# Optimization experiments

Measured on AMD Instinct MI355X. Metric: run time of the kernel, lower is better.

The kernel has to match this reference:

```python
import jax, jax.numpy as jnp
import numpy as np

B, L, D, H, NL, F = 64, 197, 768, 12, 12, 3072
HD = D // H
EPS = 1e-6


def setup_inputs() -> dict:
    key = jax.random.key(0)
    ks = jax.random.split(key, 8)
    s = 0.02  # init std, matches nn.Parameter normal_(std=0.02) / xavier-ish scale
    def n(k, shape, scale=s):
        return jax.random.normal(k, shape, jnp.float32) * scale
    return {
        "x": jax.random.normal(ks[0], (B, L, D), jnp.float32),
        "pos_emb": n(ks[1], (1, L, D)),
        "ln1_g": jnp.ones((NL, D), jnp.float32),
        "ln1_b": jnp.zeros((NL, D), jnp.float32),
        "Wq": n(ks[2], (NL, D, D)), "bq": jnp.zeros((NL, D), jnp.float32),
        "Wk": n(ks[3], (NL, D, D)), "bk": jnp.zeros((NL, D), jnp.float32),
        "Wv": n(ks[4], (NL, D, D)), "bv": jnp.zeros((NL, D), jnp.float32),
        "Wo": n(ks[5], (NL, D, D)), "bo": jnp.zeros((NL, D), jnp.float32),
        "ln2_g": jnp.ones((NL, D), jnp.float32),
        "ln2_b": jnp.zeros((NL, D), jnp.float32),
        "W1": n(ks[6], (NL, D, F)), "b1": jnp.zeros((NL, F), jnp.float32),
        "W2": n(ks[7], (NL, F, D)), "b2": jnp.zeros((NL, D), jnp.float32),
        "lnf_g": jnp.ones((D,), jnp.float32),
        "lnf_b": jnp.zeros((D,), jnp.float32),
    }


def _ln(x, g, b):
    m = jnp.mean(x, axis=-1, keepdims=True)
    v = jnp.var(x, axis=-1, keepdims=True)
    return (x - m) * jax.lax.rsqrt(v + EPS) * g + b


def reference(x, pos_emb, ln1_g, ln1_b, Wq, bq, Wk, bk, Wv, bv, Wo, bo,
              ln2_g, ln2_b, W1, b1, W2, b2, lnf_g, lnf_b):
    Bv, Lv, Dv = x.shape
    nh = H
    hd = Dv // nh
    scale = 1.0 / np.sqrt(hd).astype(np.float32)

    def block(h, p):
        g1, be1, wq, bq_, wk, bk_, wv, bv_, wo, bo_, g2, be2, w1, bb1, w2, bb2 = p
        y = _ln(h, g1, be1)
        q = (y @ wq + bq_).reshape(Bv, Lv, nh, hd)
        k = (y @ wk + bk_).reshape(Bv, Lv, nh, hd)
        v = (y @ wv + bv_).reshape(Bv, Lv, nh, hd)
        scores = jnp.einsum('bqhd,bkhd->bhqk', q, k) * scale  # [B,H,L,L]
        a = jax.nn.softmax(scores, axis=-1)
        o = jnp.einsum('bhqk,bkhd->bqhd', a, v).reshape(Bv, Lv, Dv)
        h = h + (o @ wo + bo_)
        y = _ln(h, g2, be2)
        y = jax.nn.gelu(y @ w1 + bb1, approximate=False)
        y = y @ w2 + bb2
        return h + y, None

    params = (ln1_g, ln1_b, Wq, bq, Wk, bk, Wv, bv, Wo, bo,
              ln2_g, ln2_b, W1, b1, W2, b2)
    h = x + pos_emb
    h, _ = jax.lax.scan(block, h, params)
    return _ln(h, lnf_g, lnf_b)
```

## Files before the change

kernel.cpp:

```cpp
#include <hip/hip_runtime.h>
#include <hip/hip_bf16.h>
#include <cmath>

#define B_ 64
#define L_ 197
#define D_ 768
#define H_ 12
#define NL_ 12
#define F_ 3072
#define M_ (B_*L_)
#define MPAD_ 12672

typedef __bf16 bf16_t;
typedef __bf16 bf16x8 __attribute__((ext_vector_type(8)));
typedef __bf16 bf16x4 __attribute__((ext_vector_type(4)));
typedef float  f32x4  __attribute__((ext_vector_type(4)));

#define GPTR(p) ((const __attribute__((address_space(1))) void*)(p))
#define LPTR(p) ((__attribute__((address_space(3))) void*)(p))

__device__ __forceinline__ float gelu_f(float x) {
    return 0.5f * x * (1.f + erff(x * 0.70710678118654752440f));
}

__global__ __launch_bounds__(256) void k_addpos4(const float4* __restrict__ x,
                                                 const float4* __restrict__ pos,
                                                 float4* __restrict__ h,
                                                 int n4, int ld4) {
    int i = blockIdx.x * 256 + threadIdx.x;
    if (i < n4) {
        float4 a = x[i];
        float4 p = pos[i % ld4];
        float4 r; r.x = a.x + p.x; r.y = a.y + p.y; r.z = a.z + p.z; r.w = a.w + p.w;
        h[i] = r;
    }
}

__global__ __launch_bounds__(256) void k_convT(const float* __restrict__ W,
                                               bf16_t* __restrict__ BT,
                                               int K, int N) {
    __shared__ bf16_t s[64][72];
    int tid = threadIdx.x;
    int k0 = blockIdx.x * 64, n0 = blockIdx.y * 64;
    int kr = tid >> 4, nc = (tid & 15) * 4;
    #pragma unroll
    for (int i = 0; i < 4; ++i) {
        float4 v = *(const float4*)(W + (size_t)(k0 + kr + i*16) * N + n0 + nc);
        s[kr + i*16][nc]     = (bf16_t)v.x;
        s[kr + i*16][nc + 1] = (bf16_t)v.y;
        s[kr + i*16][nc + 2] = (bf16_t)v.z;
        s[kr + i*16][nc + 3] = (bf16_t)v.w;
    }
    __syncthreads();
    int nr = tid >> 3, kc = (tid & 7) * 8;
    #pragma unroll
    for (int i = 0; i < 2; ++i) {
        bf16x8 o;
        #pragma unroll
        for (int j = 0; j < 8; ++j) o[j] = s[kc + j][nr + i*32];
        *(bf16x8*)(BT + (size_t)(n0 + nr + i*32) * K + k0 + kc) = o;
    }
}

__global__ __launch_bounds__(256) void k_pack_qkvb(const float* __restrict__ bq,
                                                   const float* __restrict__ bk,
                                                   const float* __restrict__ bv,
                                                   float* __restrict__ bqkv) {
    int i = blockIdx.x * 256 + threadIdx.x;
    if (i < D_) { bqkv[i] = bq[i]; bqkv[D_ + i] = bk[i]; bqkv[2*D_ + i] = bv[i]; }
}

template<bool BF16OUT>
__global__ __launch_bounds__(256) void k_ln(const float* __restrict__ x,
                                            const float* __restrict__ g,
                                            const float* __restrict__ bsh,
                                            void* __restrict__ out) {
    int wid = threadIdx.x >> 6, lane = threadIdx.x & 63;
    size_t row = (size_t)blockIdx.x * 4 + wid;
    const float4* xr = (const float4*)(x + row * D_);
    float4 v[3];
    float s = 0.f, sq = 0.f;
    #pragma unroll
    for (int i = 0; i < 3; ++i) {
        v[i] = xr[i*64 + lane];
        s  += v[i].x + v[i].y + v[i].z + v[i].w;
        sq += v[i].x*v[i].x + v[i].y*v[i].y + v[i].z*v[i].z + v[i].w*v[i].w;
    }
    #pragma unroll
    for (int o = 1; o < 64; o <<= 1) { s += __shfl_xor(s, o); sq += __shfl_xor(sq, o); }
    float mean = s * (1.f/768.f);
    float var  = sq * (1.f/768.f) - mean*mean;
    float rstd = rsqrtf(var + 1e-6f);
    const float4* g4 = (const float4*)g;
    const float4* b4 = (const float4*)bsh;
    #pragma unroll
    for (int i = 0; i < 3; ++i) {
        float4 gg = g4[i*64 + lane], bb = b4[i*64 + lane];
        float4 r;
        r.x = (v[i].x - mean)*rstd*gg.x + bb.x;
        r.y = (v[i].y - mean)*rstd*gg.y + bb.y;
        r.z = (v[i].z - mean)*rstd*gg.z + bb.z;
        r.w = (v[i].w - mean)*rstd*gg.w + bb.w;
        if (BF16OUT) {
            bf16x4 o4; o4[0]=(bf16_t)r.x; o4[1]=(bf16_t)r.y; o4[2]=(bf16_t)r.z; o4[3]=(bf16_t)r.w;
            ((bf16x4*)((bf16_t*)out + row * D_))[i*64 + lane] = o4;
        } else {
            ((float4*)out)[row * (D_/4) + i*64 + lane] = r;
        }
    }
}

template<int EPI>
__global__ __launch_bounds__(256, 3) void k_gemm_bt(
        const bf16_t* __restrict__ A, const bf16_t* __restrict__ BT,
        const float* __restrict__ bias, const float* __restrict__ resid,
        void* __restrict__ Cout, int K, int N, int NB) {
    __shared__ bf16_t As[128 * 64];
    __shared__ bf16_t Bs[128 * 64];

    const int tid = threadIdx.x, lane = tid & 63, wid = tid >> 6;
    const int g = lane >> 4, fr = lane & 15;
    const int wm = (wid >> 1) * 64, wn = (wid & 1) * 64;

    int nwg = (int)gridDim.x, orig = (int)blockIdx.x;
    int qq = nwg >> 3, rr = nwg & 7;
    int xcd = orig & 7, idx = orig >> 3;
    int wg = (xcd < rr ? xcd * (qq + 1) : rr * (qq + 1) + (xcd - rr) * qq) + idx;
    int bx = wg / NB, by = wg - bx * NB;
    const int gm0 = bx * 128, gn0 = by * 128;

    const int srl = lane >> 3;
    const int sc = ((lane & 7) ^ srl) * 8;

    f32x4 acc[4][4];
    #pragma unroll
    for (int i = 0; i < 4; ++i)
        #pragma unroll
        for (int j = 0; j < 4; ++j) acc[i][j] = (f32x4){0.f, 0.f, 0.f, 0.f};

    const bf16_t* a_src = A  + (size_t)(gm0 + wid * 32 + srl) * K + sc;
    const bf16_t* b_src = BT + (size_t)(gn0 + wid * 32 + srl) * K + sc;

    const int NT = K >> 6;
    for (int t = 0; t < NT; ++t) {
        const int k0 = t * 64;
        __syncthreads();
        #pragma unroll
        for (int i = 0; i < 4; ++i) {
            __builtin_amdgcn_global_load_lds(GPTR(a_src + (size_t)(i * 8) * K + k0),
                                             LPTR(&As[(wid * 32 + i * 8) * 64]), 16, 0, 0);
            __builtin_amdgcn_global_load_lds(GPTR(b_src + (size_t)(i * 8) * K + k0),
                                             LPTR(&Bs[(wid * 32 + i * 8) * 64]), 16, 0, 0);
        }
        __syncthreads();

        bf16x8 af[4][2], bf[4][2];
        #pragma unroll
        for (int mi = 0; mi < 4; ++mi) {
            const int row = wm + mi * 16 + fr;
            #pragma unroll
            for (int kc = 0; kc < 2; ++kc)
                af[mi][kc] = *(const bf16x8*)&As[row * 64 + (((kc * 4 + g) ^ (row & 7)) * 8)];
        }
        #pragma unroll
        for (int ni = 0; ni < 4; ++ni) {
            const int row = wn + ni * 16 + fr;
            #pragma unroll
            for (int kc = 0; kc < 2; ++kc)
                bf[ni][kc] = *(const bf16x8*)&Bs[row * 64 + (((kc * 4 + g) ^ (row & 7)) * 8)];
        }
        #pragma unroll
        for (int kc = 0; kc < 2; ++kc)
            #pragma unroll
            for (int mi = 0; mi < 4; ++mi)
                #pragma unroll
                for (int ni = 0; ni < 4; ++ni)
                    acc[mi][ni] = __builtin_amdgcn_mfma_f32_16x16x32_bf16(
                        af[mi][kc], bf[ni][kc], acc[mi][ni], 0, 0, 0);
    }

    const int crow = gm0 + wm + g * 4;
    const int ccol = gn0 + wn + fr;
    #pragma unroll
    for (int mi = 0; mi < 4; ++mi)
        #pragma unroll
        for (int ni = 0; ni < 4; ++ni) {
            const int c = ccol + ni * 16;
            const float bval = bias[c];
            #pragma unroll
            for (int v = 0; v < 4; ++v) {
                const int rw = crow + mi * 16 + v;
                if (rw < M_) {
                    float val = acc[mi][ni][v] + bval;
                    if (EPI == 1) val = gelu_f(val);
                    if (EPI == 2) {
                        ((float*)Cout)[(size_t)rw * N + c] = val + resid[(size_t)rw * N + c];
                    } else {
                        ((bf16_t*)Cout)[(size_t)rw * N + c] = (bf16_t)val;
                    }
                }
            }
        }
}

__global__ __launch_bounds__(256) void k_attn(const bf16_t* __restrict__ qkv,
                                              bf16_t* __restrict__ out) {
    __shared__ bf16_t VT[64][232];
    __shared__ bf16_t P[4][16][232];
    int tid = threadIdx.x, lane = tid & 63, wid = tid >> 6;
    int b = blockIdx.x / H_, hh = blockIdx.x % H_;
    const size_t base = (size_t)b * L_ * 2304 + hh * 64;

    for (int r = tid >> 3; r < L_; r += 32) {
        int cg = (tid & 7) * 8;
        bf16x8 vv = *(const bf16x8*)(qkv + base + (size_t)r * 2304 + 1536 + cg);
        #pragma unroll
        for (int j = 0; j < 8; ++j) VT[cg + j][r] = vv[j];
    }
    for (int i = tid; i < 64 * 35; i += 256) VT[i / 35][197 + i % 35] = (bf16_t)0.f;
    {
        int r = lane & 15, c0 = 208 + (lane >> 4) * 4;
        #pragma unroll
        for (int j = 0; j < 4; ++j) P[wid][r][c0 + j] = (bf16_t)0.f;
    }
    __syncthreads();

    for (int s = wid; s < 13; s += 4) {
        int q0 = s * 16;
        int qr = q0 + (lane & 15); if (qr > L_ - 1) qr = L_ - 1;
        bf16x8 qf[2];
        #pragma unroll
        for (int kk = 0; kk < 2; ++kk)
            qf[kk] = *(const bf16x8*)(qkv + base + (size_t)qr * 2304 + kk * 32 + (lane >> 4) * 8);

        f32x4 sacc[13];
        #pragma unroll
        for (int nb = 0; nb < 13; ++nb) { f32x4 z = {0.f,0.f,0.f,0.f}; sacc[nb] = z; }
        #pragma unroll
        for (int nb = 0; nb < 13; ++nb) {
            int lk = nb * 16 + (lane & 15); if (lk > L_ - 1) lk = L_ - 1;
            #pragma unroll
            for (int kk = 0; kk < 2; ++kk) {
                bf16x8 kf = *(const bf16x8*)(qkv + base + (size_t)lk * 2304 + D_ + kk * 32 + (lane >> 4) * 8);
                sacc[nb] = __builtin_amdgcn_mfma_f32_16x16x32_bf16(qf[kk], kf, sacc[nb], 0, 0, 0);
            }
        }

        float mx[4] = {-1e30f, -1e30f, -1e30f, -1e30f};
        float pv[13][4];
        #pragma unroll
        for (int nb = 0; nb < 13; ++nb) {
            bool valid = (nb * 16 + (lane & 15)) < L_;
            #pragma unroll
            for (int v = 0; v < 4; ++v) {
                float sv = valid ? sacc[nb][v] * 0.125f : -1e30f;
                pv[nb][v] = sv;
                mx[v] = fmaxf(mx[v], sv);
            }
        }
        #pragma unroll
        for (int o = 1; o < 16; o <<= 1) {
            #pragma unroll
            for (int v = 0; v < 4; ++v) mx[v] = fmaxf(mx[v], __shfl_xor(mx[v], o));
        }
        float sum[4] = {0.f, 0.f, 0.f, 0.f};
        #pragma unroll
        for (int nb = 0; nb < 13; ++nb) {
            bool valid = (nb * 16 + (lane & 15)) < L_;
            #pragma unroll
            for (int v = 0; v < 4; ++v) {
                float e2 = valid ? __expf(pv[nb][v] - mx[v]) : 0.f;
                pv[nb][v] = e2; sum[v] += e2;
            }
        }
        #pragma unroll
        for (int o = 1; o < 16; o <<= 1) {
            #pragma unroll
            for (int v = 0; v < 4; ++v) sum[v] += __shfl_xor(sum[v], o);
        }

        #pragma unroll
        for (int nb = 0; nb < 13; ++nb)
            #pragma unroll
            for (int v = 0; v < 4; ++v)
                P[wid][(lane >> 4) * 4 + v][nb * 16 + (lane & 15)] = (bf16_t)pv[nb][v];
        asm volatile("s_waitcnt lgkmcnt(0)" ::: "memory");

        f32x4 oacc[4];
        #pragma unroll
        for (int nb = 0; nb < 4; ++nb) { f32x4 z = {0.f,0.f,0.f,0.f}; oacc[nb] = z; }
        #pragma unroll
        for (int kk = 0; kk < 7; ++kk) {
            bf16x8 pf = *(const bf16x8*)&P[wid][lane & 15][kk * 32 + (lane >> 4) * 8];
            #pragma unroll
            for (int nb = 0; nb < 4; ++nb) {
                bf16x8 vf = *(const bf16x8*)&VT[nb * 16 + (lane & 15)][kk * 32 + (lane >> 4) * 8];
                oacc[nb] = __builtin_amdgcn_mfma_f32_16x16x32_bf16(pf, vf, oacc[nb], 0, 0, 0);
            }
        }

        float rs[4];
        #pragma unroll
        for (int v = 0; v < 4; ++v) rs[v] = 1.f / sum[v];
        #pragma unroll
        for (int nb = 0; nb < 4; ++nb)
            #pragma unroll
            for (int v = 0; v < 4; ++v) {
                int r = q0 + (lane >> 4) * 4 + v;
                if (r < L_)
                    out[((size_t)b * L_ + r) * D_ + hh * 64 + nb * 16 + (lane & 15)] =
                        (bf16_t)(oacc[nb][v] * rs[v]);
            }
    }
}

extern "C" void kernel_launch(void* const* d_in, const int* in_sizes, int n_in,
                              void* d_out, int out_size, void* d_ws, size_t ws_size,
                              hipStream_t stream) {
    const float* x     = (const float*)d_in[0];
    const float* pos   = (const float*)d_in[1];
    const float* ln1_g = (const float*)d_in[2];
    const float* ln1_b = (const float*)d_in[3];
    const float* Wq    = (const float*)d_in[4];
    const float* bq    = (const float*)d_in[5];
    const float* Wk    = (const float*)d_in[6];
    const float* bk    = (const float*)d_in[7];
    const float* Wv    = (const float*)d_in[8];
    const float* bv    = (const float*)d_in[9];
    const float* Wo    = (const float*)d_in[10];
    const float* bo    = (const float*)d_in[11];
    const float* ln2_g = (const float*)d_in[12];
    const float* ln2_b = (const float*)d_in[13];
    const float* W1    = (const float*)d_in[14];
    const float* b1    = (const float*)d_in[15];
    const float* W2    = (const float*)d_in[16];
    const float* b2    = (const float*)d_in[17];
    const float* lnf_g = (const float*)d_in[18];
    const float* lnf_b = (const float*)d_in[19];

    char* wsp = (char*)d_ws;
    size_t off = 0;
    auto alloc = [&](size_t bytes) -> void* {
        void* r = wsp + off;
        off += (bytes + 255) & ~(size_t)255;
        return r;
    };
    float*  h     = (float*) alloc((size_t)M_ * D_ * 4);
    bf16_t* y     = (bf16_t*)alloc((size_t)MPAD_ * D_ * 2);
    bf16_t* qkv   = (bf16_t*)alloc((size_t)M_ * 2304 * 2);
    bf16_t* attn  = (bf16_t*)alloc((size_t)MPAD_ * D_ * 2);
    bf16_t* u     = (bf16_t*)alloc((size_t)MPAD_ * F_ * 2);
    bf16_t* wqkvT = (bf16_t*)alloc((size_t)2304 * D_ * 2);
    bf16_t* woT   = (bf16_t*)alloc((size_t)D_ * D_ * 2);
    bf16_t* w1T   = (bf16_t*)alloc((size_t)F_ * D_ * 2);
    bf16_t* w2T   = (bf16_t*)alloc((size_t)D_ * F_ * 2);
    float*  bqkv  = (float*) alloc(2304 * 4);
    (void)ws_size; (void)in_sizes; (void)n_in; (void)out_size;

    {
        int n4 = M_ * D_ / 4;
        k_addpos4<<<(n4 + 255) / 256, 256, 0, stream>>>((const float4*)x, (const float4*)pos,
                                                        (float4*)h, n4, L_ * D_ / 4);
    }

    dim3 tDD (D_ / 64, D_ / 64);
    dim3 tDF (D_ / 64, F_ / 64);
    dim3 tFD (F_ / 64, D_ / 64);

    for (int l = 0; l < NL_; ++l) {
        k_convT<<<tDD, 256, 0, stream>>>(Wq + (size_t)l * D_ * D_, wqkvT,                     D_, D_);
        k_convT<<<tDD, 256, 0, stream>>>(Wk + (size_t)l * D_ * D_, wqkvT + (size_t)768 * D_,  D_, D_);
        k_convT<<<tDD, 256, 0, stream>>>(Wv + (size_t)l * D_ * D_, wqkvT + (size_t)1536 * D_, D_, D_);
        k_convT<<<tDD, 256, 0, stream>>>(Wo + (size_t)l * D_ * D_, woT, D_, D_);
        k_convT<<<tDF, 256, 0, stream>>>(W1 + (size_t)l * D_ * F_, w1T, D_, F_);
        k_convT<<<tFD, 256, 0, stream>>>(W2 + (size_t)l * F_ * D_, w2T, F_, D_);
        k_pack_qkvb<<<3, 256, 0, stream>>>(bq + l * D_, bk + l * D_, bv + l * D_, bqkv);

        k_ln<true><<<M_ / 4, 256, 0, stream>>>(h, ln1_g + l * D_, ln1_b + l * D_, y);
        k_gemm_bt<0><<<dim3(99 * 18), 256, 0, stream>>>(y,    wqkvT, bqkv,                nullptr, qkv, D_, 2304, 18);
        k_attn<<<B_ * H_, 256, 0, stream>>>(qkv, attn);
        k_gemm_bt<2><<<dim3(99 * 6),  256, 0, stream>>>(attn, woT,   bo + l * D_,         h,       h,   D_, D_,   6);
        k_ln<true><<<M_ / 4, 256, 0, stream>>>(h, ln2_g + l * D_, ln2_b + l * D_, y);
        k_gemm_bt<1><<<dim3(99 * 24), 256, 0, stream>>>(y,    w1T,   b1 + (size_t)l * F_, nullptr, u,   D_, F_,   24);
        k_gemm_bt<2><<<dim3(99 * 6),  256, 0, stream>>>(u,    w2T,   b2 + l * D_,         h,       h,   F_, D_,   6);
    }
    k_ln<false><<<M_ / 4, 256, 0, stream>>>(h, lnf_g, lnf_b, d_out);
}
```

Measured before the change: 4.371 ms.

## Add 256x128-tile GEMM for QKV and FC1, fuse weight prep launches

Adds a 512-thread GEMM kernel with 256x128 output tiles (8 waves, each computing 64x64) for the QKV and FC1 projections. The larger tile raises reuse of the A operand per loaded B tile and halves the number of workgroups. The seven per-layer weight transpose and bias pack launches become one combined k_prep launch, cutting launch overhead. MPAD is enlarged to 12800 so the 256-row tiles stay within the padded activation buffers. The larger LDS footprint and register use may lower occupancy.

```diff
diff --git a/kernel.cpp b/kernel.cpp
--- a/kernel.cpp
+++ b/kernel.cpp
@@ -9,7 +9,7 @@
 #define NL_ 12
 #define F_ 3072
 #define M_ (B_*L_)
-#define MPAD_ 12672
+#define MPAD_ 12800
 
 typedef __bf16 bf16_t;
 typedef __bf16 bf16x8 __attribute__((ext_vector_type(8)));
@@ -36,12 +36,35 @@
     }
 }
 
-__global__ __launch_bounds__(256) void k_convT(const float* __restrict__ W,
-                                               bf16_t* __restrict__ BT,
-                                               int K, int N) {
+__global__ __launch_bounds__(256) void k_prep(
+        const float* __restrict__ Wq, const float* __restrict__ Wk,
+        const float* __restrict__ Wv, const float* __restrict__ Wo,
+        const float* __restrict__ W1, const float* __restrict__ W2,
+        const float* __restrict__ bq, const float* __restrict__ bk,
+        const float* __restrict__ bv,
+        bf16_t* __restrict__ wqkvT, bf16_t* __restrict__ woT,
+        bf16_t* __restrict__ w1T, bf16_t* __restrict__ w2T,
+        float* __restrict__ bqkv) {
+    int bidx = blockIdx.x;
+    if (bidx < 3) {
+        int i = bidx * 256 + threadIdx.x;
+        if (i < D_) { bqkv[i] = bq[i]; bqkv[D_ + i] = bk[i]; bqkv[2*D_ + i] = bv[i]; }
+        return;
+    }
+    int t = bidx - 3;
+    const float* W; bf16_t* BT; int K, N;
+    if (t < 576) {
+        int seg = t / 144; t -= seg * 144;
+        K = D_; N = D_;
+        W  = (seg == 0 ? Wq : seg == 1 ? Wk : seg == 2 ? Wv : Wo);
+        BT = (seg == 3 ? woT : wqkvT + (size_t)seg * 768 * D_);
+    } else if (t < 1152) { t -= 576;  W = W1; BT = w1T; K = D_; N = F_; }
+    else                 { t -= 1152; W = W2; BT = w2T; K = F_; N = D_; }
+    const int kt = K / 64;
+    const int k0 = (t % kt) * 64, n0 = (t / kt) * 64;
+
     __shared__ bf16_t s[64][72];
     int tid = threadIdx.x;
-    int k0 = blockIdx.x * 64, n0 = blockIdx.y * 64;
     int kr = tid >> 4, nc = (tid & 15) * 4;
     #pragma unroll
     for (int i = 0; i < 4; ++i) {
@@ -60,14 +83,6 @@
         for (int j = 0; j < 8; ++j) o[j] = s[kc + j][nr + i*32];
         *(bf16x8*)(BT + (size_t)(n0 + nr + i*32) * K + k0 + kc) = o;
     }
-}
-
-__global__ __launch_bounds__(256) void k_pack_qkvb(const float* __restrict__ bq,
-                                                   const float* __restrict__ bk,
-                                                   const float* __restrict__ bv,
-                                                   float* __restrict__ bqkv) {
-    int i = blockIdx.x * 256 + threadIdx.x;
-    if (i < D_) { bqkv[i] = bq[i]; bqkv[D_ + i] = bk[i]; bqkv[2*D_ + i] = bv[i]; }
 }
 
 template<bool BF16OUT>
@@ -152,6 +167,100 @@
             __builtin_amdgcn_global_load_lds(GPTR(b_src + (size_t)(i * 8) * K + k0),
                                              LPTR(&Bs[(wid * 32 + i * 8) * 64]), 16, 0, 0);
         }
+        __syncthreads();
+
+        bf16x8 af[4][2], bf[4][2];
+        #pragma unroll
+        for (int mi = 0; mi < 4; ++mi) {
+            const int row = wm + mi * 16 + fr;
+            #pragma unroll
+            for (int kc = 0; kc < 2; ++kc)
+                af[mi][kc] = *(const bf16x8*)&As[row * 64 + (((kc * 4 + g) ^ (row & 7)) * 8)];
+        }
+        #pragma unroll
+        for (int ni = 0; ni < 4; ++ni) {
+            const int row = wn + ni * 16 + fr;
+            #pragma unroll
+            for (int kc = 0; kc < 2; ++kc)
+                bf[ni][kc] = *(const bf16x8*)&Bs[row * 64 + (((kc * 4 + g) ^ (row & 7)) * 8)];
+        }
+        #pragma unroll
+        for (int kc = 0; kc < 2; ++kc)
+            #pragma unroll
+            for (int mi = 0; mi < 4; ++mi)
+                #pragma unroll
+                for (int ni = 0; ni < 4; ++ni)
+                    acc[mi][ni] = __builtin_amdgcn_mfma_f32_16x16x32_bf16(
+                        af[mi][kc], bf[ni][kc], acc[mi][ni], 0, 0, 0);
+    }
+
+    const int crow = gm0 + wm + g * 4;
+    const int ccol = gn0 + wn + fr;
+    #pragma unroll
+    for (int mi = 0; mi < 4; ++mi)
+        #pragma unroll
+        for (int ni = 0; ni < 4; ++ni) {
+            const int c = ccol + ni * 16;
+            const float bval = bias[c];
+            #pragma unroll
+            for (int v = 0; v < 4; ++v) {
+                const int rw = crow + mi * 16 + v;
+                if (rw < M_) {
+                    float val = acc[mi][ni][v] + bval;
+                    if (EPI == 1) val = gelu_f(val);
+                    if (EPI == 2) {
+                        ((float*)Cout)[(size_t)rw * N + c] = val + resid[(size_t)rw * N + c];
+                    } else {
+                        ((bf16_t*)Cout)[(size_t)rw * N + c] = (bf16_t)val;
+                    }
+                }
+            }
+        }
+}
+
+template<int EPI>
+__global__ __launch_bounds__(512, 2) void k_gemm_big(
+        const bf16_t* __restrict__ A, const bf16_t* __restrict__ BT,
+        const float* __restrict__ bias, const float* __restrict__ resid,
+        void* __restrict__ Cout, int K, int N, int NB) {
+    __shared__ bf16_t As[256 * 64];
+    __shared__ bf16_t Bs[128 * 64];
+
+    const int tid = threadIdx.x, lane = tid & 63, wid = tid >> 6;
+    const int g = lane >> 4, fr = lane & 15;
+    const int wm = (wid >> 1) * 64, wn = (wid & 1) * 64;
+
+    int nwg = (int)gridDim.x, orig = (int)blockIdx.x;
+    int qq = nwg >> 3, rr = nwg & 7;
+    int xcd = orig & 7, idx = orig >> 3;
+    int wg = (xcd < rr ? xcd * (qq + 1) : rr * (qq + 1) + (xcd - rr) * qq) + idx;
+    int bx = wg / NB, by = wg - bx * NB;
+    const int gm0 = bx * 256, gn0 = by * 128;
+
+    const int srl = lane >> 3;
+    const int sc = ((lane & 7) ^ srl) * 8;
+
+    f32x4 acc[4][4];
+    #pragma unroll
+    for (int i = 0; i < 4; ++i)
+        #pragma unroll
+        for (int j = 0; j < 4; ++j) acc[i][j] = (f32x4){0.f, 0.f, 0.f, 0.f};
+
+    const bf16_t* a_src = A  + (size_t)(gm0 + wid * 32 + srl) * K + sc;
+    const bf16_t* b_src = BT + (size_t)(gn0 + wid * 16 + srl) * K + sc;
+
+    const int NT = K >> 6;
+    for (int t = 0; t < NT; ++t) {
+        const int k0 = t * 64;
+        __syncthreads();
+        #pragma unroll
+        for (int i = 0; i < 4; ++i)
+            __builtin_amdgcn_global_load_lds(GPTR(a_src + (size_t)(i * 8) * K + k0),
+                                             LPTR(&As[(wid * 32 + i * 8) * 64]), 16, 0, 0);
+        #pragma unroll
+        for (int i = 0; i < 2; ++i)
+            __builtin_amdgcn_global_load_lds(GPTR(b_src + (size_t)(i * 8) * K + k0),
+                                             LPTR(&Bs[(wid * 16 + i * 8) * 64]), 16, 0, 0);
         __syncthreads();
 
         bf16x8 af[4][2], bf[4][2];
@@ -363,25 +472,19 @@
                                                         (float4*)h, n4, L_ * D_ / 4);
     }
 
-    dim3 tDD (D_ / 64, D_ / 64);
-    dim3 tDF (D_ / 64, F_ / 64);
-    dim3 tFD (F_ / 64, D_ / 64);
-
     for (int l = 0; l < NL_; ++l) {
-        k_convT<<<tDD, 256, 0, stream>>>(Wq + (size_t)l * D_ * D_, wqkvT,                     D_, D_);
-        k_convT<<<tDD, 256, 0, stream>>>(Wk + (size_t)l * D_ * D_, wqkvT + (size_t)768 * D_,  D_, D_);
-        k_convT<<<tDD, 256, 0, stream>>>(Wv + (size_t)l * D_ * D_, wqkvT + (size_t)1536 * D_, D_, D_);
-        k_convT<<<tDD, 256, 0, stream>>>(Wo + (size_t)l * D_ * D_, woT, D_, D_);
-        k_convT<<<tDF, 256, 0, stream>>>(W1 + (size_t)l * D_ * F_, w1T, D_, F_);
-        k_convT<<<tFD, 256, 0, stream>>>(W2 + (size_t)l * F_ * D_, w2T, F_, D_);
-        k_pack_qkvb<<<3, 256, 0, stream>>>(bq + l * D_, bk + l * D_, bv + l * D_, bqkv);
+        k_prep<<<1731, 256, 0, stream>>>(Wq + (size_t)l * D_ * D_, Wk + (size_t)l * D_ * D_,
+                                         Wv + (size_t)l * D_ * D_, Wo + (size_t)l * D_ * D_,
+                                         W1 + (size_t)l * D_ * F_, W2 + (size_t)l * F_ * D_,
+                                         bq + l * D_, bk + l * D_, bv + l * D_,
+                                         wqkvT, woT, w1T, w2T, bqkv);
 
         k_ln<true><<<M_ / 4, 256, 0, stream>>>(h, ln1_g + l * D_, ln1_b + l * D_, y);
-        k_gemm_bt<0><<<dim3(99 * 18), 256, 0, stream>>>(y,    wqkvT, bqkv,                nullptr, qkv, D_, 2304, 18);
+        k_gemm_big<0><<<dim3(50 * 18), 512, 0, stream>>>(y,    wqkvT, bqkv,                nullptr, qkv, D_, 2304, 18);
         k_attn<<<B_ * H_, 256, 0, stream>>>(qkv, attn);
         k_gemm_bt<2><<<dim3(99 * 6),  256, 0, stream>>>(attn, woT,   bo + l * D_,         h,       h,   D_, D_,   6);
         k_ln<true><<<M_ / 4, 256, 0, stream>>>(h, ln2_g + l * D_, ln2_b + l * D_, y);
-        k_gemm_bt<1><<<dim3(99 * 24), 256, 0, stream>>>(y,    w1T,   b1 + (size_t)l * F_, nullptr, u,   D_, F_,   24);
+        k_gemm_big<1><<<dim3(50 * 24), 512, 0, stream>>>(y,    w1T,   b1 + (size_t)l * F_, nullptr, u,   D_, F_,   24);
         k_gemm_bt<2><<<dim3(99 * 6),  256, 0, stream>>>(u,    w2T,   b2 + l * D_,         h,       h,   F_, D_,   6);
     }
     k_ln<false><<<M_ / 4, 256, 0, stream>>>(h, lnf_g, lnf_b, d_out);
```

Result: faster. 4.156 ms (-4.9%).
